# Performance work log

Hardware: AMD Instinct MI355X
Metric: run time of the kernel (lower is better)

## Reference

```python
import jax, jax.numpy as jnp
import numpy as np

B, T, C = 8, 2048, 512

def setup_inputs() -> dict:
    key = jax.random.key(0)
    ks = jax.random.split(key, 16)
    def n(k, shape, s=0.02):
        return jax.random.normal(k, shape, dtype=jnp.float32) * s
    inp = {
        'x_l': jax.random.normal(ks[0], (B, T, C), jnp.float32),
        'x_r': jax.random.normal(ks[1], (B, T, C), jnp.float32),
    }
    i = 2
    for name in ['lp1', 'rp1', 'lp2', 'rp2']:
        inp[name + '_w1'] = n(ks[i], (C, C))       # pointwise conv1d weight (out,in)
        inp[name + '_b1'] = jnp.zeros((C,), jnp.float32)
        inp[name + '_w2'] = n(ks[i + 1], (C, 3))   # depthwise conv k=3 weight per channel
        inp[name + '_b2'] = jnp.zeros((C,), jnp.float32)
        i += 2
    inp['lp3_w'] = n(ks[i], (C, C)); inp['lp3_b'] = jnp.zeros((C,), jnp.float32)
    inp['rp3_w'] = n(ks[i + 1], (C, C)); inp['rp3_b'] = jnp.zeros((C,), jnp.float32)
    return inp

def _proj(x, w1, b1, w2, b2):
    # x: (B,T,C). Pointwise conv1d (1x1) then depthwise conv1d k=3, pad=1 over T.
    h = jnp.einsum('btc,dc->btd', x, w1) + b1
    hp = jnp.pad(h, ((0, 0), (1, 1), (0, 0)))
    # cross-correlation: tap 0 -> t-1, tap 1 -> t, tap 2 -> t+1 (matches torch Conv1d)
    return hp[:, :-2, :] * w2[:, 0] + hp[:, 1:-1, :] * w2[:, 1] + hp[:, 2:, :] * w2[:, 2] + b2

def reference(x_l, x_r,
              lp1_w1, lp1_b1, lp1_w2, lp1_b2,
              rp1_w1, rp1_b1, rp1_w2, rp1_b2,
              lp2_w1, lp2_b1, lp2_w2, lp2_b2,
              rp2_w1, rp2_b1, rp2_w2, rp2_b2,
              lp3_w, lp3_b, rp3_w, rp3_b):
    scale = C ** (-0.5)
    Q_l = _proj(x_l, lp1_w1, lp1_b1, lp1_w2, lp1_b2)  # (B,T,C)
    Q_r = _proj(x_r, rp1_w1, rp1_b1, rp1_w2, rp1_b2)  # (B,T,C)
    V_l = _proj(x_l, lp2_w1, lp2_b1, lp2_w2, lp2_b2)  # (B,T,C)
    V_r = _proj(x_r, rp2_w1, rp2_b1, rp2_w2, rp2_b2)  # (B,T,C)
    attn = jnp.einsum('btc,bsc->bts', Q_l, Q_r) * scale  # shared (B,T,T) scores
    # r->l: softmax over r-positions (last axis)
    F_r2l = jnp.einsum('bts,bsc->btc', jax.nn.softmax(attn, axis=-1), V_r)
    # l->r: softmax of attn^T over its last axis == softmax over axis 1 of attn
    F_l2r = jnp.einsum('bts,btc->bsc', jax.nn.softmax(attn, axis=1), V_l)
    out_l = x_l + jnp.einsum('btc,dc->btd', F_r2l, lp3_w) + lp3_b
    out_r = x_r + jnp.einsum('btc,dc->btd', F_l2r, rp3_w) + rp3_b
    return (out_l, out_r)
```

## Files before the change

kernel.cpp:

```cpp
#include <hip/hip_runtime.h>
#include <stdint.h>

#define Bb 8
#define Tt 2048
#define Cc 512

typedef __attribute__((ext_vector_type(8))) short short8;
typedef __attribute__((ext_vector_type(4))) short short4v;
typedef __attribute__((ext_vector_type(4))) float f32x4;

#define SZE ((size_t)Bb * Tt * Cc)

__device__ __forceinline__ float b2f(short s) {
  unsigned int x = ((unsigned int)(unsigned short)s) << 16;
  return __builtin_bit_cast(float, x);
}
__device__ __forceinline__ short f2b(float f) {
  unsigned int x = __builtin_bit_cast(unsigned int, f);
  x += 0x7fffu + ((x >> 16) & 1u);
  return (short)(x >> 16);
}

template<int MODE>
__global__ __launch_bounds__(256, 2)
void gemm_bt(const void* __restrict__ Av, const void* __restrict__ Av2,
             const void* __restrict__ Bv, const void* __restrict__ Bv2,
             void* __restrict__ Cv, void* __restrict__ Cv2,
             const float* __restrict__ bias,
             const float* __restrict__ resid, const float* __restrict__ resid2,
             short* __restrict__ ET, float* __restrict__ sumR, float* __restrict__ sumC,
             int M, int N, int K,
             long long sA, long long sB, long long sC, float scale)
{
  __shared__ __align__(16) short ldsA[8 * 128 * 8];
  __shared__ __align__(16) short ldsB[8 * 128 * 8];
  const int tid  = threadIdx.x;
  const int lane = tid & 63;

  int bxi = blockIdx.x, byi = blockIdx.y, bzi = blockIdx.z;
  const int gx = gridDim.x, gy = gridDim.y;
  if ((gy & 7) == 0) {
    int l = bxi + gx * (byi + gy * bzi);
    const int xcd = l & 7;
    int loc = l >> 3;
    const int ych = gy >> 3;
    bxi = loc % gx;  loc /= gx;
    byi = xcd * ych + (loc % ych);
    bzi = loc / ych;
  }

  const int bm = byi * 128;
  const int bn = bxi * 128;
  int dir = 0, zz = bzi;
  if constexpr (MODE == 1 || MODE == 2) { dir = bzi >> 3; zz = bzi & 7; }
  const long long zoA = (long long)zz * sA;
  const long long zoB = (long long)zz * sB;
  const long long zoC = (long long)zz * sC;
  const void* Ause = Av;
  const void* Buse = Bv;
  void* Cuse = Cv;
  if constexpr (MODE == 0) {
    if (zz) Ause = Av2;
  }
  if constexpr (MODE == 1 || MODE == 2) {
    if (dir) { Ause = Av2; Buse = Bv2; Cuse = Cv2; }
  }

  const int wv = tid >> 6;
  const int wm = (wv >> 1) << 6;
  const int wn = (wv & 1) << 6;

  f32x4 zero4 = {0.f, 0.f, 0.f, 0.f};
  f32x4 acc[4][4];
#pragma unroll
  for (int i = 0; i < 4; ++i)
#pragma unroll
    for (int j = 0; j < 4; ++j)
      acc[i][j] = zero4;

  const int sm  = tid >> 3;
  const int skc = tid & 7;

  for (int k0 = 0; k0 < K; k0 += 64) {
#pragma unroll
    for (int r = 0; r < 4; ++r) {
      const int m = r * 32 + sm;
      short8 av, bv;
      if constexpr (MODE == 0) {
        const float* ap = (const float*)Ause + zoA + (size_t)(bm + m) * K + k0 + skc * 8;
        float4 f0 = *(const float4*)ap;
        float4 f1 = *(const float4*)(ap + 4);
        av[0] = f2b(f0.x); av[1] = f2b(f0.y); av[2] = f2b(f0.z); av[3] = f2b(f0.w);
        av[4] = f2b(f1.x); av[5] = f2b(f1.y); av[6] = f2b(f1.z); av[7] = f2b(f1.w);
      } else {
        av = *(const short8*)((const short*)Ause + zoA + (size_t)(bm + m) * K + k0 + skc * 8);
      }
      bv = *(const short8*)((const short*)Buse + zoB + (size_t)(bn + m) * K + k0 + skc * 8);
      const int di = ((skc << 7) + (m ^ skc)) << 3;
      *(short8*)&ldsA[di] = av;
      *(short8*)&ldsB[di] = bv;
    }
    __syncthreads();
#pragma unroll
    for (int kk = 0; kk < 2; ++kk) {
      const int kcr = (kk << 2) + (lane >> 4);
      short8 af[4], bfv[4];
#pragma unroll
      for (int i = 0; i < 4; ++i) {
        const int ma = wm + i * 16 + (lane & 15);
        const int nb = wn + i * 16 + (lane & 15);
        af[i]  = *(const short8*)&ldsA[((kcr << 7) + (ma ^ kcr)) << 3];
        bfv[i] = *(const short8*)&ldsB[((kcr << 7) + (nb ^ kcr)) << 3];
      }
#pragma unroll
      for (int i = 0; i < 4; ++i)
#pragma unroll
        for (int j = 0; j < 4; ++j)
          acc[i][j] = __builtin_amdgcn_mfma_f32_16x16x32_bf16(af[i], bfv[j], acc[i][j], 0, 0, 0);
    }
    __syncthreads();
  }

  if constexpr (MODE == 4) {
#pragma unroll
    for (int i = 0; i < 4; ++i)
#pragma unroll
      for (int j = 0; j < 4; ++j)
#pragma unroll
        for (int r = 0; r < 4; ++r)
          acc[i][j][r] = __expf(acc[i][j][r] * scale);

#pragma unroll
    for (int i = 0; i < 4; ++i) {
      const int row0 = bm + wm + i * 16 + ((lane >> 4) << 2);
#pragma unroll
      for (int j = 0; j < 4; ++j) {
        const int n = bn + wn + j * 16 + (lane & 15);
        short4v t;
#pragma unroll
        for (int r = 0; r < 4; ++r) t[r] = f2b(acc[i][j][r]);
#pragma unroll
        for (int r = 0; r < 4; ++r)
          ((short*)Cv)[zoC + (size_t)(row0 + r) * N + n] = t[r];
        *(short4v*)(ET + zoC + (size_t)n * M + row0) = t;
      }
    }
#pragma unroll
    for (int i = 0; i < 4; ++i) {
      const int row0 = bm + wm + i * 16 + ((lane >> 4) << 2);
#pragma unroll
      for (int r = 0; r < 4; ++r) {
        float p = acc[i][0][r] + acc[i][1][r] + acc[i][2][r] + acc[i][3][r];
#pragma unroll
        for (int o = 1; o < 16; o <<= 1) p += __shfl_xor(p, o, 64);
        if ((lane & 15) == 0)
          unsafeAtomicAdd(&sumR[(size_t)zz * M + row0 + r], p);
      }
    }
#pragma unroll
    for (int j = 0; j < 4; ++j) {
      const int n = bn + wn + j * 16 + (lane & 15);
      float q = 0.f;
#pragma unroll
      for (int i = 0; i < 4; ++i)
#pragma unroll
        for (int r = 0; r < 4; ++r) q += acc[i][j][r];
      q += __shfl_xor(q, 16, 64);
      q += __shfl_xor(q, 32, 64);
      if (lane < 16)
        unsafeAtomicAdd(&sumC[(size_t)zz * N + n], q);
    }
  } else if constexpr (MODE == 2) {
    const float* sums = dir ? sumC : sumR;
    const float* xr   = dir ? resid2 : resid;
#pragma unroll
    for (int i = 0; i < 4; ++i) {
      const int row0 = bm + wm + i * 16 + ((lane >> 4) << 2);
#pragma unroll
      for (int r = 0; r < 4; ++r) {
        const float iv = 1.0f / sums[(size_t)zz * M + row0 + r];
#pragma unroll
        for (int j = 0; j < 4; ++j) {
          const int n = bn + wn + j * 16 + (lane & 15);
          const size_t off = zoC + (size_t)(row0 + r) * N + n;
          ((float*)Cuse)[off] = acc[i][j][r] * iv + bias[dir * N + n] + xr[off];
        }
      }
    }
  } else {
#pragma unroll
    for (int i = 0; i < 4; ++i) {
      const int row0 = bm + wm + i * 16 + ((lane >> 4) << 2);
#pragma unroll
      for (int j = 0; j < 4; ++j) {
        const int n = bn + wn + j * 16 + (lane & 15);
        float badd = 0.f;
        if (MODE == 0) badd = bias[(size_t)zz * N + n];
#pragma unroll
        for (int r = 0; r < 4; ++r) {
          float val = acc[i][j][r];
          if (MODE == 1) val *= scale;
          if (MODE == 0) val += badd;
          ((short*)Cuse)[zoC + (size_t)(row0 + r) * N + n] = f2b(val);
        }
      }
    }
  }
  (void)resid; (void)resid2; (void)ET; (void)sumR; (void)sumC;
  (void)bias; (void)scale; (void)Cuse;
}

__global__ __launch_bounds__(256)
void pack_all(const float* __restrict__ lw1a, const float* __restrict__ lw1b,
              const float* __restrict__ rw1a, const float* __restrict__ rw1b,
              const float* __restrict__ w3lf, const float* __restrict__ w3rf,
              const float* __restrict__ lb1a, const float* __restrict__ lb1b,
              const float* __restrict__ rb1a, const float* __restrict__ rb1b,
              const float* __restrict__ b3l, const float* __restrict__ b3r,
              short* __restrict__ Wl, short* __restrict__ Wr,
              short* __restrict__ W3l, short* __restrict__ W3r,
              float* __restrict__ BL, float* __restrict__ BR,
              float* __restrict__ B3, float* __restrict__ SUM)
{
  const int i = blockIdx.x * 256 + threadIdx.x;
  if (i < 524288) {
    Wl[i] = f2b(i < 262144 ? lw1a[i] : lw1b[i - 262144]);
  } else if (i < 1048576) {
    const int j = i - 524288;
    Wr[j] = f2b(j < 262144 ? rw1a[j] : rw1b[j - 262144]);
  } else if (i < 1310720) {
    W3l[i - 1048576] = f2b(w3lf[i - 1048576]);
  } else if (i < 1572864) {
    W3r[i - 1310720] = f2b(w3rf[i - 1310720]);
  } else if (i < 1573888) {
    const int j = i - 1572864;
    BL[j] = j < 512 ? lb1a[j] : lb1b[j - 512];
  } else if (i < 1574912) {
    const int j = i - 1573888;
    BR[j] = j < 512 ? rb1a[j] : rb1b[j - 512];
  } else if (i < 1575936) {
    const int j = i - 1574912;
    B3[j] = j < 512 ? b3l[j] : b3r[j - 512];
  } else if (i < 1608704) {
    SUM[i - 1575936] = 0.f;
  }
}

__global__ __launch_bounds__(256)
void dw_kernel(const short* __restrict__ H, long long hStride,
               const float* __restrict__ w2a, const float* __restrict__ w2b,
               const float* __restrict__ w2c, const float* __restrict__ w2d,
               const float* __restrict__ b2a, const float* __restrict__ b2b,
               const float* __restrict__ b2c, const float* __restrict__ b2d,
               short* __restrict__ out)
{
  const int y = blockIdx.y;
  const short* Hd = H + (size_t)(y & 1) * hStride;
  const float* w2 = (y == 0) ? w2a : (y == 1) ? w2b : (y == 2) ? w2c : w2d;
  const float* b2 = (y == 0) ? b2a : (y == 1) ? b2b : (y == 2) ? b2c : b2d;
  const int colOff = (y & 2) ? 512 : 0;
  short* outd = out + (size_t)y * SZE;

  const int idx = blockIdx.x * 256 + threadIdx.x;
  const int c8 = idx & 63;
  const int bt = idx >> 6;
  const int t  = bt & (Tt - 1);
  const int c  = c8 << 3;
  const short* base = Hd + (size_t)bt * 1024 + colOff + c;
  short8 zv = {0, 0, 0, 0, 0, 0, 0, 0};
  short8 hm = zv, hp = zv;
  short8 h0 = *(const short8*)base;
  if (t > 0)      hm = *(const short8*)(base - 1024);
  if (t < Tt - 1) hp = *(const short8*)(base + 1024);
  short8 o;
#pragma unroll
  for (int j = 0; j < 8; ++j) {
    const int cj = c + j;
    float val = b2f(hm[j]) * w2[cj * 3 + 0]
              + b2f(h0[j]) * w2[cj * 3 + 1]
              + b2f(hp[j]) * w2[cj * 3 + 2]
              + b2[cj];
    o[j] = f2b(val);
  }
  *(short8*)(outd + (size_t)bt * Cc + c) = o;
}

extern "C" void kernel_launch(void* const* d_in, const int* in_sizes, int n_in,
                              void* d_out, int out_size, void* d_ws, size_t ws_size,
                              hipStream_t stream)
{
  const float* x_l    = (const float*)d_in[0];
  const float* x_r    = (const float*)d_in[1];
  const float* lp1_w1 = (const float*)d_in[2];
  const float* lp1_b1 = (const float*)d_in[3];
  const float* lp1_w2 = (const float*)d_in[4];
  const float* lp1_b2 = (const float*)d_in[5];
  const float* rp1_w1 = (const float*)d_in[6];
  const float* rp1_b1 = (const float*)d_in[7];
  const float* rp1_w2 = (const float*)d_in[8];
  const float* rp1_b2 = (const float*)d_in[9];
  const float* lp2_w1 = (const float*)d_in[10];
  const float* lp2_b1 = (const float*)d_in[11];
  const float* lp2_w2 = (const float*)d_in[12];
  const float* lp2_b2 = (const float*)d_in[13];
  const float* rp2_w1 = (const float*)d_in[14];
  const float* rp2_b1 = (const float*)d_in[15];
  const float* rp2_w2 = (const float*)d_in[16];
  const float* rp2_b2 = (const float*)d_in[17];
  const float* lp3_w  = (const float*)d_in[18];
  const float* lp3_b  = (const float*)d_in[19];
  const float* rp3_w  = (const float*)d_in[20];
  const float* rp3_b  = (const float*)d_in[21];

  short* ws = (short*)d_ws;
  const size_t SZ = SZE;
  short* Ql   = ws;
  short* Qr   = ws + SZ;
  short* Vl   = ws + 2 * SZ;
  short* Vr   = ws + 3 * SZ;
  short* E    = ws + 4 * SZ;
  short* ETb  = ws + 8 * SZ;
  short* H    = E;
  short* VWT0 = Ql;
  short* VWT1 = Qr;

  const size_t W_PAIR = 524288, W_SING = 262144;
  short* Wl  = ws + 12 * SZ;
  short* Wr  = Wl + W_PAIR;
  short* W3l = Wr + W_PAIR;
  short* W3r = W3l + W_SING;
  float* BL  = (float*)(W3r + W_SING);
  float* BR  = BL + 1024;
  float* B3  = BR + 1024;
  float* SUMR = B3 + 1024;
  float* SUMC = SUMR + 16384;

  const float scale = 0.04419417382415922f;
  const int MT = Bb * Tt;
  const long long sQ = (long long)Tt * Cc;
  const long long sS = (long long)Tt * Tt;

  dim3 blk(256);

  pack_all<<<6284, blk, 0, stream>>>(lp1_w1, lp2_w1, rp1_w1, rp2_w1, lp3_w, rp3_w,
                                     lp1_b1, lp2_b1, rp1_b1, rp2_b1, lp3_b, rp3_b,
                                     Wl, Wr, W3l, W3r, BL, BR, B3, SUMR);

  gemm_bt<0><<<dim3(8, 128, 2), blk, 0, stream>>>(
      x_l, x_r, Wl, nullptr, H, nullptr, BL, nullptr, nullptr,
      nullptr, nullptr, nullptr,
      MT, 1024, Cc, 0, (long long)W_PAIR, (long long)(2 * SZ), 1.f);
  dw_kernel<<<dim3(4096, 4), blk, 0, stream>>>(
      H, (long long)(2 * SZ),
      lp1_w2, rp1_w2, lp2_w2, rp2_w2,
      lp1_b2, rp1_b2, lp2_b2, rp2_b2, Ql);

  gemm_bt<4><<<dim3(Tt / 128, Tt / 128, Bb), blk, 0, stream>>>(
      Ql, nullptr, Qr, nullptr, E, nullptr, nullptr, nullptr, nullptr,
      ETb, SUMR, SUMC,
      Tt, Tt, Cc, sQ, sQ, sS, scale);

  gemm_bt<1><<<dim3(Tt / 128, 4, 2 * Bb), blk, 0, stream>>>(
      W3l, W3r, Vr, Vl, VWT0, VWT1, nullptr, nullptr, nullptr,
      nullptr, nullptr, nullptr,
      512, Tt, Cc, 0, sQ, (long long)(512 * Tt), 1.f);

  gemm_bt<2><<<dim3(Cc / 128, Tt / 128, 2 * Bb), blk, 0, stream>>>(
      E, ETb, VWT0, VWT1, d_out, (float*)d_out + SZ, B3, x_l, x_r,
      nullptr, SUMR, SUMC,
      Tt, Cc, Tt, sS, (long long)(512 * Tt), sQ, 1.f);

  (void)in_sizes; (void)n_in; (void)out_size; (void)ws_size;
}
```

Measured before the change: 441.6 us.

## Fuse depthwise conv into projection GEMM epilogue with boundary fixup kernel

Moves the k=3 depthwise conv over T into the MODE 0 projection GEMM epilogue. The biased tile is staged in LDS and the stencil is applied to interior rows. The two edge rows of each 128-row tile are saved to a side buffer, and a small dwfix kernel finishes them using the neighbouring tiles. This removes the write and re-read of the full bf16 H intermediate and one large kernel launch, at the cost of extra LDS use and epilogue work in the GEMM plus a tiny extra kernel.

```diff
diff --git a/kernel.cpp b/kernel.cpp
--- a/kernel.cpp
+++ b/kernel.cpp
@@ -32,8 +32,10 @@
              int M, int N, int K,
              long long sA, long long sB, long long sC, float scale)
 {
-  __shared__ __align__(16) short ldsA[8 * 128 * 8];
-  __shared__ __align__(16) short ldsB[8 * 128 * 8];
+  constexpr int LSZ = (MODE == 0) ? 17408 : 16384;
+  __shared__ __align__(16) short ldsraw[LSZ];
+  short* ldsA = ldsraw;
+  short* ldsB = ldsraw + 8192;
   const int tid  = threadIdx.x;
   const int lane = tid & 63;
 
@@ -121,7 +123,57 @@
     __syncthreads();
   }
 
-  if constexpr (MODE == 4) {
+  if constexpr (MODE == 0) {
+#pragma unroll
+    for (int i = 0; i < 4; ++i) {
+      const int r0 = wm + i * 16 + ((lane >> 4) << 2);
+#pragma unroll
+      for (int j = 0; j < 4; ++j) {
+        const int cl = wn + j * 16 + (lane & 15);
+        const float badd = bias[(size_t)zz * N + bn + cl];
+#pragma unroll
+        for (int r = 0; r < 4; ++r)
+          ldsraw[(r0 + r) * 136 + cl] = f2b(acc[i][j][r] + badd);
+      }
+    }
+    __syncthreads();
+    const int half = bn >> 9;
+    short* outd = (short*)Cv + (size_t)(half * 2 + zz) * SZE;
+    const int cbase = bn & 511;
+    const int tl0 = tid >> 4;
+    const int c0  = (tid & 15) << 3;
+    float w0[8], w1[8], w2[8], bb[8];
+#pragma unroll
+    for (int jj = 0; jj < 8; ++jj) {
+      const int gc = zz * 1024 + bn + c0 + jj;
+      w0[jj] = resid[gc * 3 + 0];
+      w1[jj] = resid[gc * 3 + 1];
+      w2[jj] = resid[gc * 3 + 2];
+      bb[jj] = resid2[gc];
+    }
+    const size_t sidebase = (((size_t)zz * 128 + (bm >> 7)) * 4) * 1024 + bn + c0;
+#pragma unroll
+    for (int p = 0; p < 8; ++p) {
+      const int rl = p * 16 + tl0;
+      const int rm = rl == 0 ? 0 : rl - 1;
+      const int rq = rl == 127 ? 127 : rl + 1;
+      short8 hm = *(const short8*)&ldsraw[rm * 136 + c0];
+      short8 h0 = *(const short8*)&ldsraw[rl * 136 + c0];
+      short8 hp = *(const short8*)&ldsraw[rq * 136 + c0];
+      if (rl >= 1 && rl <= 126) {
+        short8 o;
+#pragma unroll
+        for (int jj = 0; jj < 8; ++jj)
+          o[jj] = f2b(b2f(hm[jj]) * w0[jj] + b2f(h0[jj]) * w1[jj]
+                      + b2f(hp[jj]) * w2[jj] + bb[jj]);
+        *(short8*)&outd[(size_t)(bm + rl) * 512 + cbase + c0] = o;
+      }
+      if (rl <= 1 || rl >= 126) {
+        const int sl = (rl >= 126) ? rl - 124 : rl;
+        *(short8*)&ET[sidebase + (size_t)sl * 1024] = h0;
+      }
+    }
+  } else if constexpr (MODE == 4) {
 #pragma unroll
     for (int i = 0; i < 4; ++i)
 #pragma unroll
@@ -194,20 +246,57 @@
 #pragma unroll
       for (int j = 0; j < 4; ++j) {
         const int n = bn + wn + j * 16 + (lane & 15);
-        float badd = 0.f;
-        if (MODE == 0) badd = bias[(size_t)zz * N + n];
 #pragma unroll
         for (int r = 0; r < 4; ++r) {
-          float val = acc[i][j][r];
-          if (MODE == 1) val *= scale;
-          if (MODE == 0) val += badd;
+          float val = acc[i][j][r] * scale;
           ((short*)Cuse)[zoC + (size_t)(row0 + r) * N + n] = f2b(val);
         }
       }
     }
   }
   (void)resid; (void)resid2; (void)ET; (void)sumR; (void)sumC;
-  (void)bias; (void)scale; (void)Cuse;
+  (void)bias; (void)scale; (void)Cuse; (void)M;
+}
+
+__global__ __launch_bounds__(256)
+void dwfix(const short* __restrict__ Hside, const float* __restrict__ W2p,
+           const float* __restrict__ B2p, short* __restrict__ outQV)
+{
+  const int idx = blockIdx.x * 256 + threadIdx.x;
+  const int c0  = (idx & 127) << 3;
+  const int rest = idx >> 7;
+  const int e   = rest & 1;
+  const int mt  = (rest >> 1) & 127;
+  const int dir = rest >> 8;
+  const size_t sbase = (((size_t)dir * 128 + mt) * 4) * 1024 + c0;
+  short8 z8 = {0, 0, 0, 0, 0, 0, 0, 0};
+  short8 hm, h0, hp;
+  int bt;
+  if (e == 0) {
+    bt = mt * 128;
+    hm = (bt & 2047) == 0 ? z8
+       : *(const short8*)&Hside[(((size_t)dir * 128 + (mt - 1)) * 4 + 3) * 1024 + c0];
+    h0 = *(const short8*)&Hside[sbase + 0 * 1024];
+    hp = *(const short8*)&Hside[sbase + 1 * 1024];
+  } else {
+    bt = mt * 128 + 127;
+    hm = *(const short8*)&Hside[sbase + 2 * 1024];
+    h0 = *(const short8*)&Hside[sbase + 3 * 1024];
+    hp = (bt & 2047) == 2047 ? z8
+       : *(const short8*)&Hside[(((size_t)dir * 128 + (mt + 1)) * 4 + 0) * 1024 + c0];
+  }
+  const int half = c0 >> 9;
+  short* outd = outQV + (size_t)(half * 2 + dir) * SZE;
+  const int cb = c0 & 511;
+  short8 o;
+#pragma unroll
+  for (int jj = 0; jj < 8; ++jj) {
+    const int gc = dir * 1024 + c0 + jj;
+    float v = b2f(hm[jj]) * W2p[gc * 3 + 0] + b2f(h0[jj]) * W2p[gc * 3 + 1]
+            + b2f(hp[jj]) * W2p[gc * 3 + 2] + B2p[gc];
+    o[jj] = f2b(v);
+  }
+  *(short8*)&outd[(size_t)bt * 512 + cb] = o;
 }
 
 __global__ __launch_bounds__(256)
@@ -217,10 +306,15 @@
               const float* __restrict__ lb1a, const float* __restrict__ lb1b,
               const float* __restrict__ rb1a, const float* __restrict__ rb1b,
               const float* __restrict__ b3l, const float* __restrict__ b3r,
+              const float* __restrict__ lw2a, const float* __restrict__ lw2b,
+              const float* __restrict__ rw2a, const float* __restrict__ rw2b,
+              const float* __restrict__ lb2a, const float* __restrict__ lb2b,
+              const float* __restrict__ rb2a, const float* __restrict__ rb2b,
               short* __restrict__ Wl, short* __restrict__ Wr,
               short* __restrict__ W3l, short* __restrict__ W3r,
               float* __restrict__ BL, float* __restrict__ BR,
-              float* __restrict__ B3, float* __restrict__ SUM)
+              float* __restrict__ B3, float* __restrict__ SUM,
+              float* __restrict__ W2p, float* __restrict__ B2p)
 {
   const int i = blockIdx.x * 256 + threadIdx.x;
   if (i < 524288) {
@@ -243,46 +337,25 @@
     B3[j] = j < 512 ? b3l[j] : b3r[j - 512];
   } else if (i < 1608704) {
     SUM[i - 1575936] = 0.f;
-  }
-}
-
-__global__ __launch_bounds__(256)
-void dw_kernel(const short* __restrict__ H, long long hStride,
-               const float* __restrict__ w2a, const float* __restrict__ w2b,
-               const float* __restrict__ w2c, const float* __restrict__ w2d,
-               const float* __restrict__ b2a, const float* __restrict__ b2b,
-               const float* __restrict__ b2c, const float* __restrict__ b2d,
-               short* __restrict__ out)
-{
-  const int y = blockIdx.y;
-  const short* Hd = H + (size_t)(y & 1) * hStride;
-  const float* w2 = (y == 0) ? w2a : (y == 1) ? w2b : (y == 2) ? w2c : w2d;
-  const float* b2 = (y == 0) ? b2a : (y == 1) ? b2b : (y == 2) ? b2c : b2d;
-  const int colOff = (y & 2) ? 512 : 0;
-  short* outd = out + (size_t)y * SZE;
-
-  const int idx = blockIdx.x * 256 + threadIdx.x;
-  const int c8 = idx & 63;
-  const int bt = idx >> 6;
-  const int t  = bt & (Tt - 1);
-  const int c  = c8 << 3;
-  const short* base = Hd + (size_t)bt * 1024 + colOff + c;
-  short8 zv = {0, 0, 0, 0, 0, 0, 0, 0};
-  short8 hm = zv, hp = zv;
-  short8 h0 = *(const short8*)base;
-  if (t > 0)      hm = *(const short8*)(base - 1024);
-  if (t < Tt - 1) hp = *(const short8*)(base + 1024);
-  short8 o;
-#pragma unroll
-  for (int j = 0; j < 8; ++j) {
-    const int cj = c + j;
-    float val = b2f(hm[j]) * w2[cj * 3 + 0]
-              + b2f(h0[j]) * w2[cj * 3 + 1]
-              + b2f(hp[j]) * w2[cj * 3 + 2]
-              + b2[cj];
-    o[j] = f2b(val);
-  }
-  *(short8*)(outd + (size_t)bt * Cc + c) = o;
+  } else if (i < 1614848) {
+    const int j = i - 1608704;
+    const int dir = j / 3072;
+    const int rem = j - dir * 3072;
+    const int col = rem / 3;
+    const int k = rem - col * 3;
+    float v;
+    if (dir == 0) v = col < 512 ? lw2a[col * 3 + k] : lw2b[(col - 512) * 3 + k];
+    else          v = col < 512 ? rw2a[col * 3 + k] : rw2b[(col - 512) * 3 + k];
+    W2p[j] = v;
+  } else if (i < 1616896) {
+    const int j = i - 1614848;
+    const int dir = j >> 10;
+    const int col = j & 1023;
+    float v;
+    if (dir == 0) v = col < 512 ? lb2a[col] : lb2b[col - 512];
+    else          v = col < 512 ? rb2a[col] : rb2b[col - 512];
+    B2p[j] = v;
+  }
 }
 
 extern "C" void kernel_launch(void* const* d_in, const int* in_sizes, int n_in,
@@ -316,13 +389,13 @@
   const size_t SZ = SZE;
   short* Ql   = ws;
   short* Qr   = ws + SZ;
-  short* Vl   = ws + 2 * SZ;
-  short* Vr   = ws + 3 * SZ;
   short* E    = ws + 4 * SZ;
   short* ETb  = ws + 8 * SZ;
-  short* H    = E;
+  short* Hside = ETb;
   short* VWT0 = Ql;
   short* VWT1 = Qr;
+  short* Vr   = ws + 3 * SZ;
+  short* Vl   = ws + 2 * SZ;
 
   const size_t W_PAIR = 524288, W_SING = 262144;
   short* Wl  = ws + 12 * SZ;
@@ -334,6 +407,8 @@
   float* B3  = BR + 1024;
   float* SUMR = B3 + 1024;
   float* SUMC = SUMR + 16384;
+  float* W2p  = SUMC + 16384;
+  float* B2p  = W2p + 6144;
 
   const float scale = 0.04419417382415922f;
   const int MT = Bb * Tt;
@@ -342,18 +417,17 @@
 
   dim3 blk(256);
 
-  pack_all<<<6284, blk, 0, stream>>>(lp1_w1, lp2_w1, rp1_w1, rp2_w1, lp3_w, rp3_w,
+  pack_all<<<6316, blk, 0, stream>>>(lp1_w1, lp2_w1, rp1_w1, rp2_w1, lp3_w, rp3_w,
                                      lp1_b1, lp2_b1, rp1_b1, rp2_b1, lp3_b, rp3_b,
-                                     Wl, Wr, W3l, W3r, BL, BR, B3, SUMR);
+                                     lp1_w2, lp2_w2, rp1_w2, rp2_w2,
+                                     lp1_b2, lp2_b2, rp1_b2, rp2_b2,
+                                     Wl, Wr, W3l, W3r, BL, BR, B3, SUMR, W2p, B2p);
 
   gemm_bt<0><<<dim3(8, 128, 2), blk, 0, stream>>>(
-      x_l, x_r, Wl, nullptr, H, nullptr, BL, nullptr, nullptr,
-      nullptr, nullptr, nullptr,
-      MT, 1024, Cc, 0, (long long)W_PAIR, (long long)(2 * SZ), 1.f);
-  dw_kernel<<<dim3(4096, 4), blk, 0, stream>>>(
-      H, (long long)(2 * SZ),
-      lp1_w2, rp1_w2, lp2_w2, rp2_w2,
-      lp1_b2, rp1_b2, lp2_b2, rp2_b2, Ql);
+      x_l, x_r, Wl, nullptr, Ql, nullptr, BL, W2p, B2p,
+      Hside, nullptr, nullptr,
+      MT, 1024, Cc, 0, (long long)W_PAIR, 0, 1.f);
+  dwfix<<<256, blk, 0, stream>>>(Hside, W2p, B2p, Ql);
 
   gemm_bt<4><<<dim3(Tt / 128, Tt / 128, Bb), blk, 0, stream>>>(
       Ql, nullptr, Qr, nullptr, E, nullptr, nullptr, nullptr, nullptr,
```

Result: slower. 462.6 us (+4.8%).
